# Performance work log

Hardware: AMD Instinct MI355X
Metric: run time of the kernel (lower is better)

The kernel has to match this reference:

```python
import jax, jax.numpy as jnp
import numpy as np


def _knn_idx(xyz, kk):
    # faithful to knn_point: full pairwise squared L2, topk of -dist
    diff = xyz[:, None, :, :] - xyz[:, :, None, :]      # (B, Nq, Nd, 3)
    dist = jnp.sum(diff * diff, axis=-1)                # (B, Nq, Nd)
    _, idx = jax.lax.top_k(-dist, kk)                   # (B, Nq, kk)
    return idx


def setup_inputs() -> dict:
    key = jax.random.key(0)
    k1, k2, k3, k4 = jax.random.split(key, 4)
    B, N, C = 4, 4096, 64
    return {
        "xyz": jax.random.normal(k1, (B, N, 3), dtype=jnp.float32),
        "w1": jax.random.normal(k2, (C, 3), dtype=jnp.float32) * 0.1,
        "w2": jax.random.normal(k3, (C, C), dtype=jnp.float32) * 0.1,
        "w3": jax.random.normal(k4, (C, C), dtype=jnp.float32) * 0.1,
        "k": 16,
    }


def reference(xyz, w1, w2, w3, k):
    # group(xyz, None, k): knn with k+1 neighbors, drop self (index 0)
    idx = _knn_idx(xyz, k + 1)[:, :, 1:]                # (B, N, k)
    # gather neighbor coords per batch: (B, N, k, 3)
    grouped = jax.vmap(lambda pts, i: pts[i])(xyz, idx)
    grouped = grouped - xyz[:, :, None, :]              # relative coords
    x = jnp.transpose(grouped, (0, 3, 1, 2))            # (B, 3, N, k)
    # 1x1 conv stack (bias=False) as einsum contractions over channel dim
    x = jax.nn.relu(jnp.einsum("oc,bcnk->bonk", w1, x))
    x = jax.nn.relu(jnp.einsum("oc,bcnk->bonk", w2, x))
    x = jnp.einsum("oc,bcnk->bonk", w3, x)
    # max-pool over neighbor axis -> (B, C, N)
    return jnp.max(x, axis=3)
```

## Files before the change

kernel.cpp:

```cpp
#include <hip/hip_runtime.h>
#include <hip/hip_bf16.h>

#define NPTS  4096
#define BATCH 4
#define KK    16
#define CH    64
#define SURV_CAP 64

typedef __attribute__((ext_vector_type(8))) short bf16x8;
typedef __attribute__((ext_vector_type(4))) float f32x4;

__device__ __forceinline__ unsigned short bhi(float x) {
    return (unsigned short)(__float_as_uint(x) >> 16);
}
__device__ __forceinline__ unsigned short blo(float x) {
    const float h = __uint_as_float(__float_as_uint(x) & 0xffff0000u);
    return (unsigned short)(__float_as_uint(x - h) >> 16);
}
__device__ __forceinline__ unsigned pk2(unsigned short a, unsigned short b) {
    return (unsigned)a | ((unsigned)b << 16);
}

__device__ __forceinline__ float ref_dist(float px, float py, float pz,
                                          float qx, float qy, float qz) {
#pragma clang fp contract(off)
    const float dx = px - qx, dy = py - qy, dz = pz - qz;
    const float sx = dx * dx, sy = dy * dy, sz = dz * dz;
    return (sx + sy) + sz;
}

__global__ __launch_bounds__(512, 4) void knn_kernel(const float* __restrict__ xyz,
                                                     int* __restrict__ knn_idx) {
    __shared__ float2 sXY[NPTS];
    __shared__ float  sZ[NPTS];
    __shared__ int sidx[8][2][SURV_CAP];
    const int wave = threadIdx.x >> 6;
    const int lane = threadIdx.x & 63;
    const int q0 = blockIdx.x * 16 + wave * 2;
    const int b = q0 >> 12;
    const int iA = q0 & (NPTS - 1), iB = iA + 1;
    const float* xb = xyz + (size_t)b * NPTS * 3;

#pragma unroll
    for (int r = 0; r < NPTS / 512; ++r) {
        const int pt = r * 512 + threadIdx.x;
        sXY[pt] = make_float2(xb[pt * 3 + 0], xb[pt * 3 + 1]);
        sZ[pt] = xb[pt * 3 + 2];
    }
    __syncthreads();

    const float2 qaXY = sXY[iA]; const float qaz = sZ[iA];
    const float2 qbXY = sXY[iB]; const float qbz = sZ[iB];
    const float qax = qaXY.x, qay = qaXY.y;
    const float qbx = qbXY.x, qby = qbXY.y;
    const float aAx = -2.f * qax, aAy = -2.f * qay, aAz = -2.f * qaz;
    const float aBx = -2.f * qbx, aBy = -2.f * qby, aBz = -2.f * qbz;

    float mA = 3.4e38f, mB = 3.4e38f;
#pragma unroll 8
    for (int t = 0; t < 64; ++t) {
        const float2 pxy = sXY[t * 64 + lane];
        const float pz = sZ[t * 64 + lane];
        const float px = pxy.x, py = pxy.y;
        const float w = fmaf(px, px, fmaf(py, py, pz * pz));
        const float sA = fmaf(pz, aAz, fmaf(py, aAy, fmaf(px, aAx, w)));
        const float sB = fmaf(pz, aBz, fmaf(py, aBy, fmaf(px, aBx, w)));
        mA = fminf(mA, sA); mB = fminf(mB, sB);
    }

#pragma unroll
    for (int k = 2; k <= 64; k <<= 1) {
#pragma unroll
        for (int jj = k >> 1; jj > 0; jj >>= 1) {
            const float pA = __shfl_xor(mA, jj);
            const float pB = __shfl_xor(mB, jj);
            const bool tm = (((lane & jj) == 0) == ((lane & k) == 0));
            mA = ((pA < mA) == tm) ? pA : mA;
            mB = ((pB < mB) == tm) ? pB : mB;
        }
    }
    const float TA = __shfl(mA, 16) + 1e-3f;
    const float TB = __shfl(mB, 16) + 1e-3f;

    int baseA = 0, baseB = 0;
#pragma unroll 4
    for (int t = 0; t < 64; ++t) {
        const float2 pxy = sXY[t * 64 + lane];
        const float pz = sZ[t * 64 + lane];
        const float px = pxy.x, py = pxy.y;
        const float w = fmaf(px, px, fmaf(py, py, pz * pz));
        const float sA = fmaf(pz, aAz, fmaf(py, aAy, fmaf(px, aAx, w)));
        const float sB = fmaf(pz, aBz, fmaf(py, aBy, fmaf(px, aBx, w)));
        {
            const bool sv = sA <= TA;
            const unsigned long long mk = __ballot(sv);
            const int slot = baseA + __popcll(mk & ((1ull << lane) - 1ull));
            if (sv && slot < SURV_CAP) sidx[wave][0][slot] = t * 64 + lane;
            baseA += __popcll(mk);
        }
        {
            const bool sv = sB <= TB;
            const unsigned long long mk = __ballot(sv);
            const int slot = baseB + __popcll(mk & ((1ull << lane) - 1ull));
            if (sv && slot < SURV_CAP) sidx[wave][1][slot] = t * 64 + lane;
            baseB += __popcll(mk);
        }
    }

    unsigned long long keyA = ~0ull, keyB = ~0ull;
    if (lane < baseA && baseA <= SURV_CAP) {
        const int j = sidx[wave][0][lane];
        const float2 pxy = sXY[j];
        const float d = ref_dist(pxy.x, pxy.y, sZ[j], qax, qay, qaz);
        keyA = ((unsigned long long)__float_as_uint(d) << 32) | (unsigned)j;
    }
    if (lane < baseB && baseB <= SURV_CAP) {
        const int j = sidx[wave][1][lane];
        const float2 pxy = sXY[j];
        const float d = ref_dist(pxy.x, pxy.y, sZ[j], qbx, qby, qbz);
        keyB = ((unsigned long long)__float_as_uint(d) << 32) | (unsigned)j;
    }

#pragma unroll
    for (int k = 2; k <= 64; k <<= 1) {
#pragma unroll
        for (int jj = k >> 1; jj > 0; jj >>= 1) {
            const unsigned long long pA = __shfl_xor(keyA, jj);
            const unsigned long long pB = __shfl_xor(keyB, jj);
            const bool tm = (((lane & jj) == 0) == ((lane & k) == 0));
            keyA = ((pA < keyA) == tm) ? pA : keyA;
            keyB = ((pB < keyB) == tm) ? pB : keyB;
        }
    }

    auto fallback = [&](int q, float qx, float qy, float qz) {
        float dp = -1.0f; int jp = -1;
        for (int pass = 0; pass < KK + 1; ++pass) {
            float dmin = 3.4e38f; int jmin = 0x7fffffff;
            for (int t = 0; t < 64; ++t) {
                const int j = t * 64 + lane;
                const float2 pxy = sXY[j];
                const float d = ref_dist(pxy.x, pxy.y, sZ[j], qx, qy, qz);
                const bool valid = (d > dp) || (d == dp && j > jp);
                const bool less = valid && (d < dmin || (d == dmin && j < jmin));
                dmin = less ? d : dmin;
                jmin = less ? j : jmin;
            }
#pragma unroll
            for (int off = 32; off > 0; off >>= 1) {
                const float d2 = __shfl_xor(dmin, off);
                const int   j2 = __shfl_xor(jmin, off);
                if (d2 < dmin || (d2 == dmin && j2 < jmin)) { dmin = d2; jmin = j2; }
            }
            if (pass >= 1 && lane == 0) knn_idx[(size_t)q * KK + pass - 1] = jmin;
            dp = dmin; jp = jmin;
        }
    };

    if (baseA <= SURV_CAP) {
        if (lane >= 1 && lane <= KK)
            knn_idx[(size_t)q0 * KK + lane - 1] = (int)(keyA & 0xffffffffu);
    } else fallback(q0, qax, qay, qaz);
    if (baseB <= SURV_CAP) {
        if (lane >= 1 && lane <= KK)
            knn_idx[(size_t)(q0 + 1) * KK + lane - 1] = (int)(keyB & 0xffffffffu);
    } else fallback(q0 + 1, qbx, qby, qbz);
}

__global__ __launch_bounds__(256, 2) void mlp_kernel(const float* __restrict__ xyz,
                                                     const int* __restrict__ knn_idx,
                                                     const float* __restrict__ w1,
                                                     const float* __restrict__ w2,
                                                     const float* __restrict__ w3,
                                                     float* __restrict__ out) {
    __shared__ __align__(16) unsigned short w2h[64 * 64], w2l[64 * 64];
    __shared__ __align__(16) unsigned short w3h[64 * 64], w3l[64 * 64];
    __shared__ __align__(16) unsigned short cbh[4][32 * 64], cbl[4][32 * 64];
    __shared__ __align__(16) float obuf[CH][36];

    const int tid = threadIdx.x;
    const int wave = tid >> 6, lane = tid & 63;
    const int lq = lane & 15, lg = lane >> 4;
    const int bx = blockIdx.x;
    const int bb = bx >> 7;
    const int nbase = (bx & 127) * 32;
    const float* xb = xyz + (size_t)bb * NPTS * 3;

    {
        const int r = tid >> 2, kb = (tid & 3) * 16;
#pragma unroll
        for (int kp = 0; kp < 16; kp += 2) {
            const int k = kb + kp;
            const float a0 = w2[r * 64 + k], a1 = w2[r * 64 + k + 1];
            const float c0 = w3[r * 64 + k], c1 = w3[r * 64 + k + 1];
            const int byt = r * 128 + (((k >> 3) ^ (r & 7)) << 4) + (k & 7) * 2;
            *(unsigned*)((char*)w2h + byt) = pk2(bhi(a0), bhi(a1));
            *(unsigned*)((char*)w2l + byt) = pk2(blo(a0), blo(a1));
            *(unsigned*)((char*)w3h + byt) = pk2(bhi(c0), bhi(c1));
            *(unsigned*)((char*)w3l + byt) = pk2(blo(c0), blo(c1));
        }
    }

    float w1v[2][8][3];
#pragma unroll
    for (int s = 0; s < 2; ++s)
#pragma unroll
        for (int j = 0; j < 8; ++j) {
            const int k = s * 32 + lg * 8 + j;
#pragma unroll
            for (int c = 0; c < 3; ++c) w1v[s][j][c] = w1[k * 3 + c];
        }

    const int col = lane & 31;
    float gxa[4], gya[4], gza[4];
#pragma unroll
    for (int g = 0; g < 4; ++g) {
        const int n = nbase + g * 8 + wave * 2 + (col >> 4);
        const int j = knn_idx[((size_t)bb * NPTS + n) * KK + (col & 15)];
        gxa[g] = xb[j * 3 + 0] - xb[n * 3 + 0];
        gya[g] = xb[j * 3 + 1] - xb[n * 3 + 1];
        gza[g] = xb[j * 3 + 2] - xb[n * 3 + 2];
    }
    __syncthreads();

    unsigned short* const cbH = cbh[wave];
    unsigned short* const cbL = cbl[wave];

#pragma unroll
    for (int g = 0; g < 4; ++g) {
        bf16x8 b1h[2][2], b1l[2][2];
#pragma unroll
        for (int t = 0; t < 2; ++t) {
            const int src = t * 16 + lq;
            const float sgx = __shfl(gxa[g], src);
            const float sgy = __shfl(gya[g], src);
            const float sgz = __shfl(gza[g], src);
#pragma unroll
            for (int s = 0; s < 2; ++s) {
                bf16x8 hh, ll;
#pragma unroll
                for (int j = 0; j < 8; ++j) {
                    float v = fmaf(w1v[s][j][2], sgz,
                              fmaf(w1v[s][j][1], sgy, w1v[s][j][0] * sgx));
                    v = fmaxf(v, 0.f);
                    hh[j] = (short)bhi(v);
                    ll[j] = (short)blo(v);
                }
                b1h[s][t] = hh; b1l[s][t] = ll;
            }
        }

        f32x4 acc[4][2];
#pragma unroll
        for (int m = 0; m < 4; ++m)
#pragma unroll
            for (int t = 0; t < 2; ++t) acc[m][t] = (f32x4){0.f, 0.f, 0.f, 0.f};
#pragma unroll
        for (int m = 0; m < 4; ++m) {
            const int r = m * 16 + lq;
#pragma unroll
            for (int s = 0; s < 2; ++s) {
                const int byt = r * 128 + (((s * 4 + lg) ^ (r & 7)) << 4);
                const bf16x8 ah = *(const bf16x8*)((const char*)w2h + byt);
                const bf16x8 al = *(const bf16x8*)((const char*)w2l + byt);
#pragma unroll
                for (int t = 0; t < 2; ++t) {
                    acc[m][t] = __builtin_amdgcn_mfma_f32_16x16x32_bf16(ah, b1h[s][t], acc[m][t], 0, 0, 0);
                    acc[m][t] = __builtin_amdgcn_mfma_f32_16x16x32_bf16(ah, b1l[s][t], acc[m][t], 0, 0, 0);
                    acc[m][t] = __builtin_amdgcn_mfma_f32_16x16x32_bf16(al, b1h[s][t], acc[m][t], 0, 0, 0);
                }
            }
        }

#pragma unroll
        for (int m = 0; m < 4; ++m)
#pragma unroll
            for (int t = 0; t < 2; ++t) {
                f32x4 v = acc[m][t];
#pragma unroll
                for (int e = 0; e < 4; ++e) v[e] = fmaxf(v[e], 0.f);
                const int co = t * 16 + lq;
                const int k0 = m * 16 + lg * 4;
                const int byt = co * 128 + (((k0 >> 3) ^ (co & 7)) << 4) + (k0 & 7) * 2;
                uint2 hw, lw;
                hw.x = pk2(bhi(v[0]), bhi(v[1])); hw.y = pk2(bhi(v[2]), bhi(v[3]));
                lw.x = pk2(blo(v[0]), blo(v[1])); lw.y = pk2(blo(v[2]), blo(v[3]));
                *(uint2*)((char*)cbH + byt) = hw;
                *(uint2*)((char*)cbL + byt) = lw;
            }

        bf16x8 xh[2][2], xl[2][2];
#pragma unroll
        for (int s = 0; s < 2; ++s)
#pragma unroll
            for (int t = 0; t < 2; ++t) {
                const int co = t * 16 + lq;
                const int byt = co * 128 + (((s * 4 + lg) ^ (co & 7)) << 4);
                xh[s][t] = *(const bf16x8*)((const char*)cbH + byt);
                xl[s][t] = *(const bf16x8*)((const char*)cbL + byt);
            }
        f32x4 acc3[4][2];
#pragma unroll
        for (int mb = 0; mb < 4; ++mb)
#pragma unroll
            for (int t = 0; t < 2; ++t) acc3[mb][t] = (f32x4){0.f, 0.f, 0.f, 0.f};
#pragma unroll
        for (int mb = 0; mb < 4; ++mb) {
            const int r = mb * 16 + lq;
#pragma unroll
            for (int s = 0; s < 2; ++s) {
                const int byt = r * 128 + (((s * 4 + lg) ^ (r & 7)) << 4);
                const bf16x8 wh = *(const bf16x8*)((const char*)w3h + byt);
                const bf16x8 wl = *(const bf16x8*)((const char*)w3l + byt);
#pragma unroll
                for (int t = 0; t < 2; ++t) {
                    acc3[mb][t] = __builtin_amdgcn_mfma_f32_16x16x32_bf16(xh[s][t], wh, acc3[mb][t], 0, 0, 0);
                    acc3[mb][t] = __builtin_amdgcn_mfma_f32_16x16x32_bf16(xh[s][t], wl, acc3[mb][t], 0, 0, 0);
                    acc3[mb][t] = __builtin_amdgcn_mfma_f32_16x16x32_bf16(xl[s][t], wh, acc3[mb][t], 0, 0, 0);
                }
            }
        }

#pragma unroll
        for (int mb = 0; mb < 4; ++mb)
#pragma unroll
            for (int t = 0; t < 2; ++t) {
                float v = fmaxf(fmaxf(acc3[mb][t][0], acc3[mb][t][1]),
                                fmaxf(acc3[mb][t][2], acc3[mb][t][3]));
                v = fmaxf(v, __shfl_xor(v, 16));
                v = fmaxf(v, __shfl_xor(v, 32));
                if (lg == 0) obuf[mb * 16 + lq][g * 8 + wave * 2 + t] = v;
            }
    }
    __syncthreads();

    {
        const int c = tid >> 2, seg = tid & 3;
        const float4 v0 = *(const float4*)&obuf[c][seg * 8];
        const float4 v1 = *(const float4*)&obuf[c][seg * 8 + 4];
        float* op = &out[((size_t)(bb * CH + c)) * NPTS + nbase + seg * 8];
        *(float4*)op = v0;
        *(float4*)(op + 4) = v1;
    }
}

extern "C" void kernel_launch(void* const* d_in, const int* in_sizes, int n_in,
                              void* d_out, int out_size, void* d_ws, size_t ws_size,
                              hipStream_t stream) {
    (void)in_sizes; (void)n_in; (void)out_size; (void)ws_size;
    const float* xyz = (const float*)d_in[0];
    const float* w1  = (const float*)d_in[1];
    const float* w2  = (const float*)d_in[2];
    const float* w3  = (const float*)d_in[3];
    int*   knn = (int*)d_ws;
    float* out = (float*)d_out;

    knn_kernel<<<BATCH * NPTS / 16, 512, 0, stream>>>(xyz, knn);
    mlp_kernel<<<BATCH * NPTS / 32, 256, 0, stream>>>(xyz, knn, w1, w2, w3, out);
}
```

Before: 114.7 us.

## Process four queries per wave in KNN and compact survivors with LDS atomics

Each wave now handles four query points instead of two, so every point load from shared memory and the shared norm term feed four distance evaluations, and the grid is halved. Survivor compaction switches from ballot/popcount prefix sums to per-query LDS atomic counters, and the survivor cap drops from 64 to 40. This cuts shared-memory traffic and block-setup overhead per query. In exchange it raises register pressure, adds atomic contention, and makes the slow fallback path more likely when more than 40 candidates pass the threshold.

```diff
diff --git a/kernel.cpp b/kernel.cpp
--- a/kernel.cpp
+++ b/kernel.cpp
@@ -5,7 +5,7 @@
 #define BATCH 4
 #define KK    16
 #define CH    64
-#define SURV_CAP 64
+#define SURV_CAP 40
 
 typedef __attribute__((ext_vector_type(8))) short bf16x8;
 typedef __attribute__((ext_vector_type(4))) float f32x4;
@@ -33,12 +33,13 @@
                                                      int* __restrict__ knn_idx) {
     __shared__ float2 sXY[NPTS];
     __shared__ float  sZ[NPTS];
-    __shared__ int sidx[8][2][SURV_CAP];
+    __shared__ int sidx[8][4][SURV_CAP];
+    __shared__ int scnt[8][4];
     const int wave = threadIdx.x >> 6;
     const int lane = threadIdx.x & 63;
-    const int q0 = blockIdx.x * 16 + wave * 2;
+    const int q0 = blockIdx.x * 32 + wave * 4;
     const int b = q0 >> 12;
-    const int iA = q0 & (NPTS - 1), iB = iA + 1;
+    const int i0 = q0 & (NPTS - 1);
     const float* xb = xyz + (size_t)b * NPTS * 3;
 
 #pragma unroll
@@ -47,100 +48,99 @@
         sXY[pt] = make_float2(xb[pt * 3 + 0], xb[pt * 3 + 1]);
         sZ[pt] = xb[pt * 3 + 2];
     }
+    if (lane < 4) scnt[wave][lane] = 0;
     __syncthreads();
 
-    const float2 qaXY = sXY[iA]; const float qaz = sZ[iA];
-    const float2 qbXY = sXY[iB]; const float qbz = sZ[iB];
-    const float qax = qaXY.x, qay = qaXY.y;
-    const float qbx = qbXY.x, qby = qbXY.y;
-    const float aAx = -2.f * qax, aAy = -2.f * qay, aAz = -2.f * qaz;
-    const float aBx = -2.f * qbx, aBy = -2.f * qby, aBz = -2.f * qbz;
-
-    float mA = 3.4e38f, mB = 3.4e38f;
+    float qx[4], qy[4], qz[4], ax[4], ay[4], az[4];
+#pragma unroll
+    for (int v = 0; v < 4; ++v) {
+        const float2 t = sXY[i0 + v];
+        qx[v] = t.x; qy[v] = t.y; qz[v] = sZ[i0 + v];
+        ax[v] = -2.f * qx[v]; ay[v] = -2.f * qy[v]; az[v] = -2.f * qz[v];
+    }
+
+    float mn[4] = {3.4e38f, 3.4e38f, 3.4e38f, 3.4e38f};
 #pragma unroll 8
     for (int t = 0; t < 64; ++t) {
         const float2 pxy = sXY[t * 64 + lane];
         const float pz = sZ[t * 64 + lane];
         const float px = pxy.x, py = pxy.y;
         const float w = fmaf(px, px, fmaf(py, py, pz * pz));
-        const float sA = fmaf(pz, aAz, fmaf(py, aAy, fmaf(px, aAx, w)));
-        const float sB = fmaf(pz, aBz, fmaf(py, aBy, fmaf(px, aBx, w)));
-        mA = fminf(mA, sA); mB = fminf(mB, sB);
+#pragma unroll
+        for (int v = 0; v < 4; ++v) {
+            const float s = fmaf(pz, az[v], fmaf(py, ay[v], fmaf(px, ax[v], w)));
+            mn[v] = fminf(mn[v], s);
+        }
     }
 
 #pragma unroll
     for (int k = 2; k <= 64; k <<= 1) {
 #pragma unroll
         for (int jj = k >> 1; jj > 0; jj >>= 1) {
-            const float pA = __shfl_xor(mA, jj);
-            const float pB = __shfl_xor(mB, jj);
             const bool tm = (((lane & jj) == 0) == ((lane & k) == 0));
-            mA = ((pA < mA) == tm) ? pA : mA;
-            mB = ((pB < mB) == tm) ? pB : mB;
-        }
-    }
-    const float TA = __shfl(mA, 16) + 1e-3f;
-    const float TB = __shfl(mB, 16) + 1e-3f;
-
-    int baseA = 0, baseB = 0;
+#pragma unroll
+            for (int v = 0; v < 4; ++v) {
+                const float p = __shfl_xor(mn[v], jj);
+                mn[v] = ((p < mn[v]) == tm) ? p : mn[v];
+            }
+        }
+    }
+    float T[4];
+#pragma unroll
+    for (int v = 0; v < 4; ++v) T[v] = __shfl(mn[v], 16) + 1e-3f;
+
 #pragma unroll 4
     for (int t = 0; t < 64; ++t) {
         const float2 pxy = sXY[t * 64 + lane];
         const float pz = sZ[t * 64 + lane];
         const float px = pxy.x, py = pxy.y;
         const float w = fmaf(px, px, fmaf(py, py, pz * pz));
-        const float sA = fmaf(pz, aAz, fmaf(py, aAy, fmaf(px, aAx, w)));
-        const float sB = fmaf(pz, aBz, fmaf(py, aBy, fmaf(px, aBx, w)));
-        {
-            const bool sv = sA <= TA;
-            const unsigned long long mk = __ballot(sv);
-            const int slot = baseA + __popcll(mk & ((1ull << lane) - 1ull));
-            if (sv && slot < SURV_CAP) sidx[wave][0][slot] = t * 64 + lane;
-            baseA += __popcll(mk);
-        }
-        {
-            const bool sv = sB <= TB;
-            const unsigned long long mk = __ballot(sv);
-            const int slot = baseB + __popcll(mk & ((1ull << lane) - 1ull));
-            if (sv && slot < SURV_CAP) sidx[wave][1][slot] = t * 64 + lane;
-            baseB += __popcll(mk);
-        }
-    }
-
-    unsigned long long keyA = ~0ull, keyB = ~0ull;
-    if (lane < baseA && baseA <= SURV_CAP) {
-        const int j = sidx[wave][0][lane];
-        const float2 pxy = sXY[j];
-        const float d = ref_dist(pxy.x, pxy.y, sZ[j], qax, qay, qaz);
-        keyA = ((unsigned long long)__float_as_uint(d) << 32) | (unsigned)j;
-    }
-    if (lane < baseB && baseB <= SURV_CAP) {
-        const int j = sidx[wave][1][lane];
-        const float2 pxy = sXY[j];
-        const float d = ref_dist(pxy.x, pxy.y, sZ[j], qbx, qby, qbz);
-        keyB = ((unsigned long long)__float_as_uint(d) << 32) | (unsigned)j;
+#pragma unroll
+        for (int v = 0; v < 4; ++v) {
+            const float s = fmaf(pz, az[v], fmaf(py, ay[v], fmaf(px, ax[v], w)));
+            if (s <= T[v]) {
+                const int slot = atomicAdd(&scnt[wave][v], 1);
+                if (slot < SURV_CAP) sidx[wave][v][slot] = t * 64 + lane;
+            }
+        }
+    }
+    int cnt[4];
+#pragma unroll
+    for (int v = 0; v < 4; ++v) cnt[v] = scnt[wave][v];
+
+    unsigned long long key[4];
+#pragma unroll
+    for (int v = 0; v < 4; ++v) {
+        key[v] = ~0ull;
+        if (lane < cnt[v] && cnt[v] <= SURV_CAP) {
+            const int j = sidx[wave][v][lane];
+            const float2 pxy = sXY[j];
+            const float d = ref_dist(pxy.x, pxy.y, sZ[j], qx[v], qy[v], qz[v]);
+            key[v] = ((unsigned long long)__float_as_uint(d) << 32) | (unsigned)j;
+        }
     }
 
 #pragma unroll
     for (int k = 2; k <= 64; k <<= 1) {
 #pragma unroll
         for (int jj = k >> 1; jj > 0; jj >>= 1) {
-            const unsigned long long pA = __shfl_xor(keyA, jj);
-            const unsigned long long pB = __shfl_xor(keyB, jj);
             const bool tm = (((lane & jj) == 0) == ((lane & k) == 0));
-            keyA = ((pA < keyA) == tm) ? pA : keyA;
-            keyB = ((pB < keyB) == tm) ? pB : keyB;
-        }
-    }
-
-    auto fallback = [&](int q, float qx, float qy, float qz) {
+#pragma unroll
+            for (int v = 0; v < 4; ++v) {
+                const unsigned long long p = __shfl_xor(key[v], jj);
+                key[v] = ((p < key[v]) == tm) ? p : key[v];
+            }
+        }
+    }
+
+    auto fallback = [&](int q, float fqx, float fqy, float fqz) {
         float dp = -1.0f; int jp = -1;
         for (int pass = 0; pass < KK + 1; ++pass) {
             float dmin = 3.4e38f; int jmin = 0x7fffffff;
             for (int t = 0; t < 64; ++t) {
                 const int j = t * 64 + lane;
                 const float2 pxy = sXY[j];
-                const float d = ref_dist(pxy.x, pxy.y, sZ[j], qx, qy, qz);
+                const float d = ref_dist(pxy.x, pxy.y, sZ[j], fqx, fqy, fqz);
                 const bool valid = (d > dp) || (d == dp && j > jp);
                 const bool less = valid && (d < dmin || (d == dmin && j < jmin));
                 dmin = less ? d : dmin;
@@ -157,14 +157,13 @@
         }
     };
 
-    if (baseA <= SURV_CAP) {
-        if (lane >= 1 && lane <= KK)
-            knn_idx[(size_t)q0 * KK + lane - 1] = (int)(keyA & 0xffffffffu);
-    } else fallback(q0, qax, qay, qaz);
-    if (baseB <= SURV_CAP) {
-        if (lane >= 1 && lane <= KK)
-            knn_idx[(size_t)(q0 + 1) * KK + lane - 1] = (int)(keyB & 0xffffffffu);
-    } else fallback(q0 + 1, qbx, qby, qbz);
+#pragma unroll
+    for (int v = 0; v < 4; ++v) {
+        if (cnt[v] <= SURV_CAP) {
+            if (lane >= 1 && lane <= KK)
+                knn_idx[(size_t)(q0 + v) * KK + lane - 1] = (int)(key[v] & 0xffffffffu);
+        } else fallback(q0 + v, qx[v], qy[v], qz[v]);
+    }
 }
 
 __global__ __launch_bounds__(256, 2) void mlp_kernel(const float* __restrict__ xyz,
@@ -355,6 +354,6 @@
     int*   knn = (int*)d_ws;
     float* out = (float*)d_out;
 
-    knn_kernel<<<BATCH * NPTS / 16, 512, 0, stream>>>(xyz, knn);
+    knn_kernel<<<BATCH * NPTS / 32, 512, 0, stream>>>(xyz, knn);
     mlp_kernel<<<BATCH * NPTS / 32, 256, 0, stream>>>(xyz, knn, w1, w2, w3, out);
 }
```

After: 106.6 us. 1.08x faster.
